# Kernel optimization log

Hardware: AMD Instinct MI355X
Metric: run time of the kernel (lower is better)

## Reference

```python
import jax, jax.numpy as jnp
import numpy as np

D_MODEL = 1024
N_HEADS = 16
HEAD_DIM = D_MODEL // N_HEADS
D_FF = 4096
ROPE_BASE = 10000.0
LN_EPS = 1e-5


def setup_inputs() -> dict:
    key = jax.random.key(0)
    ks = jax.random.split(key, 12)
    B, S = 2, 2048
    s = 0.02
    inp = {
        "x": jax.random.normal(ks[0], (B, S, D_MODEL), dtype=jnp.float32),
        "Wq": jax.random.normal(ks[1], (D_MODEL, D_MODEL), dtype=jnp.float32) * s,
        "bq": jnp.zeros((D_MODEL,), jnp.float32),
        "Wk": jax.random.normal(ks[2], (D_MODEL, D_MODEL), dtype=jnp.float32) * s,
        "bk": jnp.zeros((D_MODEL,), jnp.float32),
        "Wv": jax.random.normal(ks[3], (D_MODEL, D_MODEL), dtype=jnp.float32) * s,
        "bv": jnp.zeros((D_MODEL,), jnp.float32),
        "Wo": jax.random.normal(ks[4], (D_MODEL, D_MODEL), dtype=jnp.float32) * s,
        "bo": jnp.zeros((D_MODEL,), jnp.float32),
        "ln1_g": jnp.ones((D_MODEL,), jnp.float32),
        "ln1_b": jnp.zeros((D_MODEL,), jnp.float32),
        "W1": jax.random.normal(ks[5], (D_MODEL, D_FF), dtype=jnp.float32) * s,
        "b1": jnp.zeros((D_FF,), jnp.float32),
        "W2": jax.random.normal(ks[6], (D_FF, D_MODEL), dtype=jnp.float32) * s,
        "b2": jnp.zeros((D_MODEL,), jnp.float32),
        "ln2_g": jnp.ones((D_MODEL,), jnp.float32),
        "ln2_b": jnp.zeros((D_MODEL,), jnp.float32),
    }
    return inp


def _layernorm(x, g, b):
    mu = jnp.mean(x, axis=-1, keepdims=True)
    var = jnp.var(x, axis=-1, keepdims=True)
    return (x - mu) * jax.lax.rsqrt(var + LN_EPS) * g + b


def _rope_cos_sin(seq_len, dtype):
    inv_freq = 1.0 / (ROPE_BASE ** (jnp.arange(0, HEAD_DIM, 2, dtype=jnp.float32) / HEAD_DIM))
    t = jnp.arange(seq_len, dtype=jnp.float32)
    freqs = jnp.einsum("i,j->ij", t, inv_freq)          # [S, HEAD_DIM/2]
    emb = jnp.concatenate([freqs, freqs], axis=-1)        # [S, HEAD_DIM]
    return jnp.cos(emb).astype(dtype), jnp.sin(emb).astype(dtype)


def _rotate_half(x):
    x1, x2 = jnp.split(x, 2, axis=-1)
    return jnp.concatenate([-x2, x1], axis=-1)


def reference(x, Wq, bq, Wk, bk, Wv, bv, Wo, bo, ln1_g, ln1_b,
              W1, b1, W2, b2, ln2_g, ln2_b):
    B, S, _ = x.shape
    residual = x
    h = _layernorm(x, ln1_g, ln1_b)

    def split_heads(y):  # [B,S,D] -> [B,H,S,hd]
        return y.reshape(B, S, N_HEADS, HEAD_DIM).transpose(0, 2, 1, 3)

    q = split_heads(h @ Wq + bq)
    k = split_heads(h @ Wk + bk)
    v = split_heads(h @ Wv + bv)

    cos, sin = _rope_cos_sin(S, x.dtype)  # [S, hd], broadcast over B,H
    q = q * cos + _rotate_half(q) * sin
    k = k * cos + _rotate_half(k) * sin

    scale = HEAD_DIM ** -0.5
    scores = jnp.einsum("bhqd,bhkd->bhqk", q, k) * scale
    attn = jax.nn.softmax(scores, axis=-1)
    ctx = jnp.einsum("bhqk,bhkd->bhqd", attn, v)           # [B,H,S,hd]
    ctx = ctx.transpose(0, 2, 1, 3).reshape(B, S, D_MODEL)
    attn_out = ctx @ Wo + bo

    x = residual + attn_out
    residual = x
    h = _layernorm(x, ln2_g, ln2_b)
    ffn = jax.nn.gelu(h @ W1 + b1, approximate=False) @ W2 + b2
    return residual + ffn
```

## Files before the change

### kernel.cpp

```cpp
#include <hip/hip_runtime.h>
#include <hip/hip_bf16.h>
#include <stdint.h>

#define S_LEN 2048
#define NH 16
#define HD 64
#define DM 1024
#define DFF 4096
#define MTOK 4096

typedef __attribute__((ext_vector_type(8))) short short8;
typedef __attribute__((ext_vector_type(4))) float f32x4;
typedef unsigned short u16;
typedef unsigned int u32;

__device__ __forceinline__ float bf2f(u16 u) {
  union { u32 i; float f; } x; x.i = ((u32)u) << 16; return x.f;
}
__device__ __forceinline__ u16 f2bf(float f) {
  union { float f; u32 i; } x; x.f = f;
  u32 r = x.i + 0x7fffu + ((x.i >> 16) & 1u);
  return (u16)(r >> 16);
}
__device__ __forceinline__ void gload16(const u16* g, u16* l) {
  __builtin_amdgcn_global_load_lds(
      (__attribute__((address_space(1))) u32*)g,
      (__attribute__((address_space(3))) u32*)l, 16, 0, 0);
}

#define VM0 asm volatile("s_waitcnt vmcnt(0)" ::: "memory")
#define VM6 asm volatile("s_waitcnt vmcnt(6)" ::: "memory")
#define BARR do { __builtin_amdgcn_s_barrier(); asm volatile("" ::: "memory"); } while (0)
#define LGKM0 do { asm volatile("s_waitcnt lgkmcnt(0)" ::: "memory"); __builtin_amdgcn_sched_barrier(0); } while (0)
#define PRIO1 __builtin_amdgcn_s_setprio(1)
#define PRIO0 __builtin_amdgcn_s_setprio(0)

__device__ __forceinline__ void transpose_tile(const float* __restrict__ W,
                                               u16* __restrict__ Wt, int K, int N,
                                               int n0, int k0, int tx, int ty,
                                               float (*tile)[33]) {
#pragma unroll
  for (int i = 0; i < 4; ++i)
    tile[ty + i * 8][tx] = W[(size_t)(k0 + ty + i * 8) * N + n0 + tx];
  __syncthreads();
#pragma unroll
  for (int i = 0; i < 4; ++i)
    Wt[(size_t)(n0 + ty + i * 8) * K + k0 + tx] = f2bf(tile[tx][ty + i * 8]);
}

__global__ __launch_bounds__(256) void prep(
    const float* __restrict__ Wq, const float* __restrict__ Wk,
    const float* __restrict__ Wv, const float* __restrict__ Wo,
    const float* __restrict__ W1, const float* __restrict__ W2,
    u16* __restrict__ WQKVT, u16* __restrict__ WOT, u16* __restrict__ W1T,
    u16* __restrict__ W2T, float* __restrict__ cosT, float* __restrict__ sinT,
    const float* __restrict__ x, const float* __restrict__ g,
    const float* __restrict__ b, u16* __restrict__ H) {
  __shared__ float tile[32][33];
  __shared__ float red[8];
  const int r = blockIdx.x;
  const int t = threadIdx.x;
  const int tx = t & 31, ty = t >> 5;
  if (r < 4096) {
    const float* W = (r < 1024) ? Wq : (r < 2048) ? Wk : (r < 3072) ? Wv : Wo;
    u16* Wt = (r < 1024) ? WQKVT
              : (r < 2048) ? WQKVT + 1024 * 1024
              : (r < 3072) ? WQKVT + 2 * 1024 * 1024 : WOT;
    int sub = r & 1023;
    transpose_tile(W, Wt, 1024, 1024, (sub & 31) * 32, (sub >> 5) * 32, tx, ty, tile);
  } else if (r < 8192) {
    int sub = r - 4096;
    transpose_tile(W1, W1T, 1024, 4096, (sub & 127) * 32, (sub >> 7) * 32, tx, ty, tile);
  } else if (r < 12288) {
    int sub = r - 8192;
    transpose_tile(W2, W2T, 4096, 1024, (sub & 31) * 32, (sub >> 5) * 32, tx, ty, tile);
  } else if (r < 12544) {
    int id = (r - 12288) * 256 + t;
    int s = id >> 5, j = id & 31;
    float inv = powf(10000.0f, -(float)j * (1.0f / 32.0f));
    float fr = (float)s * inv;
    cosT[id] = cosf(fr);
    sinT[id] = sinf(fr);
  } else {
    int row = r - 12544;
    float4 v = ((const float4*)(x + ((size_t)row << 10)))[t];
    float s = v.x + v.y + v.z + v.w;
    float q = v.x * v.x + v.y * v.y + v.z * v.z + v.w * v.w;
#pragma unroll
    for (int m = 1; m < 64; m <<= 1) {
      s += __shfl_xor(s, m, 64);
      q += __shfl_xor(q, m, 64);
    }
    int lane = t & 63, w = t >> 6;
    if (lane == 0) { red[w] = s; red[4 + w] = q; }
    __syncthreads();
    s = red[0] + red[1] + red[2] + red[3];
    q = red[4] + red[5] + red[6] + red[7];
    float mu = s * (1.0f / 1024.0f);
    float var = q * (1.0f / 1024.0f) - mu * mu;
    float rstd = rsqrtf(var + 1e-5f);
    float4 gv = ((const float4*)g)[t];
    float4 bv = ((const float4*)b)[t];
    ushort4 o;
    o.x = f2bf((v.x - mu) * rstd * gv.x + bv.x);
    o.y = f2bf((v.y - mu) * rstd * gv.y + bv.y);
    o.z = f2bf((v.z - mu) * rstd * gv.z + bv.z);
    o.w = f2bf((v.w - mu) * rstd * gv.w + bv.w);
    ((ushort4*)(H + ((size_t)row << 10)))[t] = o;
  }
}

__global__ __launch_bounds__(256) void ln_bf16(const float* __restrict__ x,
                                               const float* __restrict__ g,
                                               const float* __restrict__ b,
                                               u16* __restrict__ out) {
  int row = blockIdx.x;
  int t = threadIdx.x;
  float4 v = ((const float4*)(x + ((size_t)row << 10)))[t];
  float s = v.x + v.y + v.z + v.w;
  float q = v.x * v.x + v.y * v.y + v.z * v.z + v.w * v.w;
#pragma unroll
  for (int m = 1; m < 64; m <<= 1) {
    s += __shfl_xor(s, m, 64);
    q += __shfl_xor(q, m, 64);
  }
  __shared__ float red[8];
  int lane = t & 63, w = t >> 6;
  if (lane == 0) { red[w] = s; red[4 + w] = q; }
  __syncthreads();
  s = red[0] + red[1] + red[2] + red[3];
  q = red[4] + red[5] + red[6] + red[7];
  float mu = s * (1.0f / 1024.0f);
  float var = q * (1.0f / 1024.0f) - mu * mu;
  float rstd = rsqrtf(var + 1e-5f);
  float4 gv = ((const float4*)g)[t];
  float4 bv = ((const float4*)b)[t];
  ushort4 o;
  o.x = f2bf((v.x - mu) * rstd * gv.x + bv.x);
  o.y = f2bf((v.y - mu) * rstd * gv.y + bv.y);
  o.z = f2bf((v.z - mu) * rstd * gv.z + bv.z);
  o.w = f2bf((v.w - mu) * rstd * gv.w + bv.w);
  ((ushort4*)(out + ((size_t)row << 10)))[t] = o;
}

#define MMQ(IB, NB)                                                          \
  _Pragma("unroll") for (int i_ = 0; i_ < 4; ++i_)                           \
  _Pragma("unroll") for (int n_ = 0; n_ < 2; ++n_)                           \
  _Pragma("unroll") for (int k_ = 0; k_ < 2; ++k_)                           \
    acc[(IB) + i_][(NB) + n_] = __builtin_amdgcn_mfma_f32_16x16x32_bf16(     \
        a[i_][k_], b[(NB) + n_][k_], acc[(IB) + i_][(NB) + n_], 0, 0, 0);

template <int EPI>
__global__ __launch_bounds__(512, 2) void gemm256(
    const u16* __restrict__ A, const u16* __restrict__ Bt, int N, int K,
    const float* __restrict__ bias, const float* __restrict__ bq,
    const float* __restrict__ bk, const float* __restrict__ bv,
    const float* __restrict__ cosT, const float* __restrict__ sinT,
    u16* __restrict__ d0, u16* __restrict__ d1, u16* __restrict__ d2) {
  __shared__ __align__(16) u16 As[2][256 * 64];
  __shared__ __align__(16) u16 Bs[2][256 * 64];
  const int t = threadIdx.x;
  const int lane = t & 63, wid = t >> 6;
  const int fr = lane & 15, fq = lane >> 4;
  const int m0 = blockIdx.y << 8, n0 = blockIdx.x << 8;
  const int wmo = (wid >> 2) << 7;
  const int wno = (wid & 3) << 6;
  const int r7 = fr & 7;
  const int srow = t >> 3, ssl = t & 7;

  f32x4 acc[8][4];
#pragma unroll
  for (int i = 0; i < 8; ++i)
#pragma unroll
    for (int n = 0; n < 4; ++n) acc[i][n] = (f32x4){0.f, 0.f, 0.f, 0.f};

  short8 a[4][2], b[4][2];

  auto stageA = [&](int slot, int kt) {
#pragma unroll
    for (int c = 0; c < 4; ++c) {
      const int row = (c << 6) + srow;
      gload16(A + (size_t)(m0 + row) * K + kt + ((ssl ^ (row & 7)) << 3),
              &As[slot][(size_t)((c << 9) + t) << 3]);
    }
  };
  auto stageB = [&](int slot, int kt) {
#pragma unroll
    for (int c = 0; c < 4; ++c) {
      const int row = (c << 6) + srow;
      gload16(Bt + (size_t)(n0 + row) * K + kt + ((ssl ^ (row & 7)) << 3),
              &Bs[slot][(size_t)((c << 9) + t) << 3]);
    }
  };
  auto readA = [&](int slot, int ibase) {
#pragma unroll
    for (int i = 0; i < 4; ++i) {
      const u16* rp = &As[slot][(wmo + ((ibase + i) << 4) + fr) << 6];
      a[i][0] = *(const short8*)(rp + ((fq ^ r7) << 3));
      a[i][1] = *(const short8*)(rp + (((4 + fq) ^ r7) << 3));
    }
  };
  auto readB = [&](int slot, int nbase) {
#pragma unroll
    for (int n = 0; n < 2; ++n) {
      const u16* rp = &Bs[slot][(wno + ((nbase + n) << 4) + fr) << 6];
      b[nbase + n][0] = *(const short8*)(rp + ((fq ^ r7) << 3));
      b[nbase + n][1] = *(const short8*)(rp + (((4 + fq) ^ r7) << 3));
    }
  };

  stageA(0, 0);
  stageB(0, 0);
  const int iters = K >> 7;
  for (int it = 0; it < iters; ++it) {
    const int kt = it << 7;
    VM0; BARR;
    readA(0, 0); readB(0, 0);
    stageA(1, kt + 64);
    LGKM0; PRIO1; MMQ(0, 0); PRIO0;
    BARR;
    readB(0, 2);
    stageB(1, kt + 64);
    LGKM0; PRIO1; MMQ(0, 2); PRIO0;
    BARR;
    readA(0, 4);
    LGKM0; PRIO1; MMQ(4, 2); PRIO0;
    BARR;
    PRIO1; MMQ(4, 0); PRIO0;
    VM0; BARR;
    readA(1, 0); readB(1, 0);
    if (it + 1 < iters) stageA(0, kt + 128);
    LGKM0; PRIO1; MMQ(0, 0); PRIO0;
    BARR;
    readB(1, 2);
    if (it + 1 < iters) stageB(0, kt + 128);
    LGKM0; PRIO1; MMQ(0, 2); PRIO0;
    BARR;
    readA(1, 4);
    LGKM0; PRIO1; MMQ(4, 2); PRIO0;
    BARR;
    PRIO1; MMQ(4, 0); PRIO0;
  }

  if (EPI == 0) {
    const int colbase = n0 + wno;
    const int slice = colbase >> 10;
    const int cb = colbase & 1023;
    const int hh = cb >> 6;
    if (slice < 2) {
      const float sc = (slice == 0) ? 0.125f * 1.44269504088896f : 1.0f;
      const float* bb_ = (slice == 0) ? bq : bk;
      u16* dst = (slice == 0) ? d0 : d1;
#pragma unroll
      for (int i = 0; i < 8; ++i) {
        const int row0 = m0 + wmo + (i << 4) + (fq << 2);
#pragma unroll
        for (int n = 0; n < 2; ++n) {
          const int d = n * 16 + fr;
          const float blo = bb_[cb + d];
          const float bhi = bb_[cb + d + 32];
#pragma unroll
          for (int j = 0; j < 4; ++j) {
            const int row = row0 + j;
            const int ss = row & 2047, bb2 = row >> 11;
            const float c = cosT[ss * 32 + d];
            const float sn = sinT[ss * 32 + d];
            const float av = acc[i][n][j] + blo;
            const float bv2 = acc[i][n + 2][j] + bhi;
            const size_t base = ((size_t)((bb2 * 16 + hh) * 2048 + ss)) << 6;
            dst[base + d] = f2bf((av * c - bv2 * sn) * sc);
            dst[base + d + 32] = f2bf((bv2 * c + av * sn) * sc);
          }
        }
      }
    } else {
#pragma unroll
      for (int i = 0; i < 8; ++i) {
        const int row0 = m0 + wmo + (i << 4) + (fq << 2);
#pragma unroll
        for (int n = 0; n < 4; ++n) {
          const int d = n * 16 + fr;
          const float bia = bv[cb + d];
#pragma unroll
          for (int j = 0; j < 4; ++j) {
            const int row = row0 + j;
            const int ss = row & 2047, bb2 = row >> 11;
            d2[((size_t)((bb2 * 16 + hh) * 64 + d)) * 2048 + ss] =
                f2bf(acc[i][n][j] + bia);
          }
        }
      }
    }
  } else {
#pragma unroll
    for (int i = 0; i < 8; ++i) {
      const int row0 = m0 + wmo + (i << 4) + (fq << 2);
#pragma unroll
      for (int n = 0; n < 4; ++n) {
        const int col = n0 + wno + n * 16 + fr;
        const float bia = bias[col];
#pragma unroll
        for (int j = 0; j < 4; ++j) {
          const int row = row0 + j;
          const float v = acc[i][n][j] + bia;
          const float gl = 0.5f * v * (1.0f + erff(v * 0.70710678118f));
          d0[(size_t)row * N + col] = f2bf(gl);
        }
      }
    }
  }
}

__global__ __launch_bounds__(256, 2) void gemm_bt2(
    const u16* __restrict__ A, const u16* __restrict__ Bt, int K,
    const float* __restrict__ bias, const float* __restrict__ resid,
    float* __restrict__ dst) {
  __shared__ __align__(16) u16 As[3][128 * 64];
  __shared__ __align__(16) u16 Bs[3][64 * 64];
  const int t = threadIdx.x, lane = t & 63, wid = t >> 6;
  const int fr = lane & 15, fq = lane >> 4;
  const int bid = blockIdx.x;
  const int xcd = bid & 7, within = bid >> 3;
  const int m0 = (xcd * 4 + (within >> 4)) << 7;
  const int n0 = (within & 15) << 6;
  const int wm = (wid >> 1) << 6;
  const int wn = (wid & 1) << 5;
  const int sr = t >> 3, sl = t & 7;
  const int sw7 = fr & 7;

  f32x4 acc[4][2];
#pragma unroll
  for (int i = 0; i < 4; ++i)
#pragma unroll
    for (int n = 0; n < 2; ++n) acc[i][n] = (f32x4){0.f, 0.f, 0.f, 0.f};

  auto stage = [&](int b, int kt) {
#pragma unroll
    for (int c = 0; c < 4; ++c) {
      int R = c * 32 + sr;
      gload16(A + (size_t)(m0 + R) * K + kt + ((sl ^ (R & 7)) << 3),
              &As[b][R * 64 + sl * 8]);
    }
#pragma unroll
    for (int c = 0; c < 2; ++c) {
      int R = c * 32 + sr;
      gload16(Bt + (size_t)(n0 + R) * K + kt + ((sl ^ (R & 7)) << 3),
              &Bs[b][R * 64 + sl * 8]);
    }
  };

  stage(0, 0);
  stage(1, 64);
  const int iters = K >> 6;
  for (int it = 0; it < iters; ++it) {
    if (it + 1 < iters) { VM6; } else { VM0; }
    BARR;
    if (it + 2 < iters) stage((it + 2) % 3, (it + 2) << 6);
    const int slot = it % 3;
    short8 a[4][2], b[2][2];
#pragma unroll
    for (int i = 0; i < 4; ++i) {
      const char* rp = (const char*)&As[slot][(wm + i * 16 + fr) * 64];
      a[i][0] = *(const short8*)(rp + ((fq ^ sw7) << 4));
      a[i][1] = *(const short8*)(rp + (((4 + fq) ^ sw7) << 4));
    }
#pragma unroll
    for (int n = 0; n < 2; ++n) {
      const char* rp = (const char*)&Bs[slot][(wn + n * 16 + fr) * 64];
      b[n][0] = *(const short8*)(rp + ((fq ^ sw7) << 4));
      b[n][1] = *(const short8*)(rp + (((4 + fq) ^ sw7) << 4));
    }
    PRIO1;
#pragma unroll
    for (int i = 0; i < 4; ++i)
#pragma unroll
      for (int n = 0; n < 2; ++n)
#pragma unroll
        for (int k2 = 0; k2 < 2; ++k2)
          acc[i][n] = __builtin_amdgcn_mfma_f32_16x16x32_bf16(a[i][k2], b[n][k2],
                                                              acc[i][n], 0, 0, 0);
    PRIO0;
  }

#pragma unroll
  for (int i = 0; i < 4; ++i) {
    int row0 = m0 + wm + i * 16 + (fq << 2);
#pragma unroll
    for (int n = 0; n < 2; ++n) {
      int col = n0 + wn + n * 16 + fr;
      float bia = bias[col];
#pragma unroll
      for (int j = 0; j < 4; ++j) {
        size_t idx = (size_t)(row0 + j) * 1024 + col;
        dst[idx] = acc[i][n][j] + bia + resid[idx];
      }
    }
  }
}

__global__ __launch_bounds__(512, 4) void attn_fwd(const u16* __restrict__ q,
                                                   const u16* __restrict__ k,
                                                   const u16* __restrict__ vt,
                                                   u16* __restrict__ ctx) {
  __shared__ __align__(16) u16 Ks[2][64 * 64];
  __shared__ __align__(16) u16 Vs[2][64 * 64];
  __shared__ __align__(16) u16 Pb[8][16 * 64];
  const int t = threadIdx.x, lane = t & 63, w = t >> 6;
  const int fr = lane & 15, fq = lane >> 4;
  const int bid = blockIdx.x;
  const int bh = (bid & 7) * 4 + ((bid >> 3) & 3);
  const int qt = bid >> 5;
  const int q0w = qt * 128 + w * 16;
  const size_t hbase = (size_t)bh << 17;
  const u16* kg = k + hbase;
  const u16* vg = vt + hbase;
  const int sr = t >> 3;
  const int sl = t & 7;
  const int sw7 = fr & 7;

  short8 aq0, aq1;
  {
    const u16* qp = q + hbase + (size_t)(q0w + fr) * 64 + fq * 8;
    aq0 = *(const short8*)qp;
    aq1 = *(const short8*)(qp + 32);
  }

  float lacc = 0.f;
  f32x4 o[4];
#pragma unroll
  for (int n = 0; n < 4; ++n) o[n] = (f32x4){0.f, 0.f, 0.f, 0.f};

  auto stage = [&](int buf, int kt) {
    int gs = sl ^ (sr & 7);
    gload16(kg + (size_t)(kt + sr) * 64 + gs * 8, &Ks[buf][sr * 64 + sl * 8]);
    gload16(vg + (size_t)sr * 2048 + kt + gs * 8, &Vs[buf][sr * 64 + sl * 8]);
  };

  stage(0, 0);
  int buf = 0;
  for (int it = 0; it < 32; ++it) {
    VM0;
    BARR;
    if (it < 31) stage(buf ^ 1, (it + 1) * 64);

    f32x4 s[4];
    const char* kbase = (const char*)&Ks[buf][0];
    PRIO1;
#pragma unroll
    for (int n = 0; n < 4; ++n) {
      const char* kr = kbase + (n * 16 + fr) * 128;
      short8 kb0 = *(const short8*)(kr + ((fq ^ sw7) << 4));
      short8 kb1 = *(const short8*)(kr + (((4 + fq) ^ sw7) << 4));
      s[n] = (f32x4){0.f, 0.f, 0.f, 0.f};
      s[n] = __builtin_amdgcn_mfma_f32_16x16x32_bf16(kb0, aq0, s[n], 0, 0, 0);
      s[n] = __builtin_amdgcn_mfma_f32_16x16x32_bf16(kb1, aq1, s[n], 0, 0, 0);
    }
    PRIO0;

    char* pw = (char*)&Pb[w][0];
#pragma unroll
    for (int n = 0; n < 4; ++n) {
      float p0 = exp2f(s[n][0]);
      float p1 = exp2f(s[n][1]);
      float p2 = exp2f(s[n][2]);
      float p3 = exp2f(s[n][3]);
      lacc += (p0 + p1) + (p2 + p3);
      u32 d0, d1;
      asm volatile("v_cvt_pk_bf16_f32 %0, %1, %2" : "=v"(d0) : "v"(p0), "v"(p1));
      asm volatile("v_cvt_pk_bf16_f32 %0, %1, %2" : "=v"(d1) : "v"(p2), "v"(p3));
      int off = fr * 128 + ((n * 32 + fq * 8) ^ (sw7 << 4));
      *(uint2*)(pw + off) = make_uint2(d0, d1);
    }

    LGKM0;
    const char* prd = (const char*)&Pb[w][0];
    short8 ap0 = *(const short8*)(prd + fr * 128 + ((fq ^ sw7) << 4));
    short8 ap1 = *(const short8*)(prd + fr * 128 + (((4 + fq) ^ sw7) << 4));

    const char* vbase = (const char*)&Vs[buf][0];
    PRIO1;
#pragma unroll
    for (int n = 0; n < 4; ++n) {
      const char* vr = vbase + (n * 16 + fr) * 128;
      short8 vb0 = *(const short8*)(vr + ((fq ^ sw7) << 4));
      short8 vb1 = *(const short8*)(vr + (((4 + fq) ^ sw7) << 4));
      o[n] = __builtin_amdgcn_mfma_f32_16x16x32_bf16(ap0, vb0, o[n], 0, 0, 0);
      o[n] = __builtin_amdgcn_mfma_f32_16x16x32_bf16(ap1, vb1, o[n], 0, 0, 0);
    }
    PRIO0;
    buf ^= 1;
  }

  lacc += __shfl_xor(lacc, 16, 64);
  lacc += __shfl_xor(lacc, 32, 64);

  const int bb = bh >> 4, hh = bh & 15;
  float rl[4];
#pragma unroll
  for (int j = 0; j < 4; ++j) rl[j] = 1.0f / __shfl(lacc, fq * 4 + j, 64);
#pragma unroll
  for (int n = 0; n < 4; ++n) {
    int d = n * 16 + fr;
#pragma unroll
    for (int j = 0; j < 4; ++j) {
      int row = q0w + fq * 4 + j;
      ctx[(((size_t)(bb * 2048 + row)) << 10) + hh * 64 + d] = f2bf(o[n][j] * rl[j]);
    }
  }
}

extern "C" void kernel_launch(void* const* d_in, const int* in_sizes, int n_in,
                              void* d_out, int out_size, void* d_ws, size_t ws_size,
                              hipStream_t stream) {
  const float* x    = (const float*)d_in[0];
  const float* Wq   = (const float*)d_in[1];
  const float* bq   = (const float*)d_in[2];
  const float* Wk   = (const float*)d_in[3];
  const float* bk   = (const float*)d_in[4];
  const float* Wv   = (const float*)d_in[5];
  const float* bv   = (const float*)d_in[6];
  const float* Wo   = (const float*)d_in[7];
  const float* bo   = (const float*)d_in[8];
  const float* ln1g = (const float*)d_in[9];
  const float* ln1b = (const float*)d_in[10];
  const float* W1   = (const float*)d_in[11];
  const float* b1   = (const float*)d_in[12];
  const float* W2   = (const float*)d_in[13];
  const float* b2   = (const float*)d_in[14];
  const float* ln2g = (const float*)d_in[15];
  const float* ln2b = (const float*)d_in[16];

  char* ws = (char*)d_ws;
  size_t off = 0;
  auto alloc = [&](size_t bytes) {
    char* p = ws + off;
    off += (bytes + 1023) & ~(size_t)1023;
    return p;
  };
  u16* WQKVT = (u16*)alloc((size_t)3 * DM * DM * 2);
  u16* WOT = (u16*)alloc((size_t)DM * DM * 2);
  u16* W1T = (u16*)alloc((size_t)DFF * DM * 2);
  u16* W2T = (u16*)alloc((size_t)DM * DFF * 2);
  float* COS = (float*)alloc((size_t)S_LEN * 32 * 4);
  float* SIN = (float*)alloc((size_t)S_LEN * 32 * 4);
  u16* H   = (u16*)alloc((size_t)MTOK * DM * 2);
  u16* Qb  = (u16*)alloc((size_t)MTOK * DM * 2);
  u16* Kb  = (u16*)alloc((size_t)MTOK * DM * 2);
  u16* VT  = (u16*)alloc((size_t)MTOK * DM * 2);
  u16* CTX = (u16*)alloc((size_t)MTOK * DM * 2);
  float* X2 = (float*)alloc((size_t)MTOK * DM * 4);
  u16* FFN1 = Qb;
  if (ws_size < off) return;

  dim3 blk256(256);
  prep<<<dim3(16640), blk256, 0, stream>>>(Wq, Wk, Wv, Wo, W1, W2, WQKVT, WOT,
                                           W1T, W2T, COS, SIN, x, ln1g, ln1b, H);
  gemm256<0><<<dim3(12, 16), dim3(512), 0, stream>>>(
      H, WQKVT, 3072, 1024, nullptr, bq, bk, bv, COS, SIN, Qb, Kb, VT);
  attn_fwd<<<dim3(512), dim3(512), 0, stream>>>(Qb, Kb, VT, CTX);
  gemm_bt2<<<dim3(512), blk256, 0, stream>>>(CTX, WOT, 1024, bo, x, X2);
  ln_bf16<<<4096, blk256, 0, stream>>>(X2, ln2g, ln2b, H);
  gemm256<1><<<dim3(16, 16), dim3(512), 0, stream>>>(
      H, W1T, 4096, 1024, b1, nullptr, nullptr, nullptr, nullptr, nullptr,
      FFN1, nullptr, nullptr);
  gemm_bt2<<<dim3(512), blk256, 0, stream>>>(FFN1, W2T, 4096, b2, X2, (float*)d_out);
}
```

Before: 243.4 us.

## Rewrite attention with 32x32x16 MFMA and register-resident P via permlane32 swap

The attention kernel moves from 16x16x32 to 32x32x16 bf16 MFMA. Each wave now owns 32 query rows, and blocks shrink from 512 to 256 threads. The softmax probabilities are repacked into the A-operand layout in registers using permlane32_swap, which removes the per-wave LDS round trip for P and its wait. This is meant to cut LDS traffic and instruction count and to raise MFMA efficiency. In exchange it needs more registers per thread and puts fewer waves per block to hide the K/V staging latency.

```diff
diff --git a/kernel.cpp b/kernel.cpp
--- a/kernel.cpp
+++ b/kernel.cpp
@@ -11,6 +11,8 @@
 
 typedef __attribute__((ext_vector_type(8))) short short8;
 typedef __attribute__((ext_vector_type(4))) float f32x4;
+typedef __attribute__((ext_vector_type(16))) float f32x16;
+typedef __attribute__((ext_vector_type(2))) int i32x2;
 typedef unsigned short u16;
 typedef unsigned int u32;
 
@@ -398,42 +400,52 @@
   }
 }
 
-__global__ __launch_bounds__(512, 4) void attn_fwd(const u16* __restrict__ q,
+__global__ __launch_bounds__(256, 4) void attn_fwd(const u16* __restrict__ q,
                                                    const u16* __restrict__ k,
                                                    const u16* __restrict__ vt,
                                                    u16* __restrict__ ctx) {
   __shared__ __align__(16) u16 Ks[2][64 * 64];
   __shared__ __align__(16) u16 Vs[2][64 * 64];
-  __shared__ __align__(16) u16 Pb[8][16 * 64];
+  __shared__ float Lr[4][32];
   const int t = threadIdx.x, lane = t & 63, w = t >> 6;
-  const int fr = lane & 15, fq = lane >> 4;
+  const int ql = lane & 31;
+  const int h = lane >> 5;
   const int bid = blockIdx.x;
   const int bh = (bid & 7) * 4 + ((bid >> 3) & 3);
   const int qt = bid >> 5;
-  const int q0w = qt * 128 + w * 16;
+  const int q0w = qt * 128 + w * 32;
   const size_t hbase = (size_t)bh << 17;
   const u16* kg = k + hbase;
   const u16* vg = vt + hbase;
   const int sr = t >> 3;
   const int sl = t & 7;
-  const int sw7 = fr & 7;
-
-  short8 aq0, aq1;
-  {
-    const u16* qp = q + hbase + (size_t)(q0w + fr) * 64 + fq * 8;
-    aq0 = *(const short8*)qp;
-    aq1 = *(const short8*)(qp + 32);
-  }
+  const int l7 = lane & 7;
+
+  short8 qf[4];
+#pragma unroll
+  for (int f = 0; f < 4; ++f)
+    qf[f] = *(const short8*)(q + hbase + (size_t)(q0w + ql) * 64 + f * 16 + h * 8);
 
   float lacc = 0.f;
-  f32x4 o[4];
-#pragma unroll
-  for (int n = 0; n < 4; ++n) o[n] = (f32x4){0.f, 0.f, 0.f, 0.f};
+  f32x16 o[2];
+#pragma unroll
+  for (int db = 0; db < 2; ++db)
+#pragma unroll
+    for (int r = 0; r < 16; ++r) o[db][r] = 0.f;
 
   auto stage = [&](int buf, int kt) {
-    int gs = sl ^ (sr & 7);
-    gload16(kg + (size_t)(kt + sr) * 64 + gs * 8, &Ks[buf][sr * 64 + sl * 8]);
-    gload16(vg + (size_t)sr * 2048 + kt + gs * 8, &Vs[buf][sr * 64 + sl * 8]);
+#pragma unroll
+    for (int c = 0; c < 2; ++c) {
+      int R = c * 32 + sr;
+      int gs = sl ^ (R & 7);
+      gload16(kg + (size_t)(kt + R) * 64 + gs * 8, &Ks[buf][R * 64 + sl * 8]);
+    }
+#pragma unroll
+    for (int c = 0; c < 2; ++c) {
+      int R = c * 32 + sr;
+      int gs = sl ^ (R & 7);
+      gload16(vg + (size_t)R * 2048 + kt + gs * 8, &Vs[buf][R * 64 + sl * 8]);
+    }
   };
 
   stage(0, 0);
@@ -443,69 +455,78 @@
     BARR;
     if (it < 31) stage(buf ^ 1, (it + 1) * 64);
 
-    f32x4 s[4];
-    const char* kbase = (const char*)&Ks[buf][0];
+    f32x16 s[2];
     PRIO1;
 #pragma unroll
-    for (int n = 0; n < 4; ++n) {
-      const char* kr = kbase + (n * 16 + fr) * 128;
-      short8 kb0 = *(const short8*)(kr + ((fq ^ sw7) << 4));
-      short8 kb1 = *(const short8*)(kr + (((4 + fq) ^ sw7) << 4));
-      s[n] = (f32x4){0.f, 0.f, 0.f, 0.f};
-      s[n] = __builtin_amdgcn_mfma_f32_16x16x32_bf16(kb0, aq0, s[n], 0, 0, 0);
-      s[n] = __builtin_amdgcn_mfma_f32_16x16x32_bf16(kb1, aq1, s[n], 0, 0, 0);
+    for (int kb = 0; kb < 2; ++kb) {
+#pragma unroll
+      for (int r = 0; r < 16; ++r) s[kb][r] = 0.f;
+#pragma unroll
+      for (int f = 0; f < 4; ++f) {
+        const u16* kr = &Ks[buf][(kb * 32 + ql) * 64 + (((2 * f + h) ^ l7) << 3)];
+        s[kb] = __builtin_amdgcn_mfma_f32_32x32x16_bf16(*(const short8*)kr, qf[f],
+                                                        s[kb], 0, 0, 0);
+      }
     }
     PRIO0;
 
-    char* pw = (char*)&Pb[w][0];
-#pragma unroll
-    for (int n = 0; n < 4; ++n) {
-      float p0 = exp2f(s[n][0]);
-      float p1 = exp2f(s[n][1]);
-      float p2 = exp2f(s[n][2]);
-      float p3 = exp2f(s[n][3]);
-      lacc += (p0 + p1) + (p2 + p3);
-      u32 d0, d1;
-      asm volatile("v_cvt_pk_bf16_f32 %0, %1, %2" : "=v"(d0) : "v"(p0), "v"(p1));
-      asm volatile("v_cvt_pk_bf16_f32 %0, %1, %2" : "=v"(d1) : "v"(p2), "v"(p3));
-      int off = fr * 128 + ((n * 32 + fq * 8) ^ (sw7 << 4));
-      *(uint2*)(pw + off) = make_uint2(d0, d1);
-    }
-
-    LGKM0;
-    const char* prd = (const char*)&Pb[w][0];
-    short8 ap0 = *(const short8*)(prd + fr * 128 + ((fq ^ sw7) << 4));
-    short8 ap1 = *(const short8*)(prd + fr * 128 + (((4 + fq) ^ sw7) << 4));
-
-    const char* vbase = (const char*)&Vs[buf][0];
+    float p[2][16];
+#pragma unroll
+    for (int kb = 0; kb < 2; ++kb)
+#pragma unroll
+      for (int r = 0; r < 16; ++r) {
+        p[kb][r] = exp2f(s[kb][r]);
+        lacc += p[kb][r];
+      }
+
+    short8 pf[4];
+#pragma unroll
+    for (int kb = 0; kb < 2; ++kb)
+#pragma unroll
+      for (int rrp = 0; rrp < 2; ++rrp) {
+        u32 y0, y1, x0, x1;
+        asm volatile("v_cvt_pk_bf16_f32 %0, %1, %2" : "=v"(y0)
+                     : "v"(p[kb][8 * rrp + 0]), "v"(p[kb][8 * rrp + 1]));
+        asm volatile("v_cvt_pk_bf16_f32 %0, %1, %2" : "=v"(y1)
+                     : "v"(p[kb][8 * rrp + 2]), "v"(p[kb][8 * rrp + 3]));
+        asm volatile("v_cvt_pk_bf16_f32 %0, %1, %2" : "=v"(x0)
+                     : "v"(p[kb][8 * rrp + 4]), "v"(p[kb][8 * rrp + 5]));
+        asm volatile("v_cvt_pk_bf16_f32 %0, %1, %2" : "=v"(x1)
+                     : "v"(p[kb][8 * rrp + 6]), "v"(p[kb][8 * rrp + 7]));
+        i32x2 r0 = __builtin_amdgcn_permlane32_swap((int)x0, (int)y0, false, false);
+        i32x2 r1 = __builtin_amdgcn_permlane32_swap((int)x1, (int)y1, false, false);
+        u32 dw[4] = {(u32)r0[1], (u32)r1[1], (u32)r0[0], (u32)r1[0]};
+        pf[kb * 2 + rrp] = *(short8*)dw;
+      }
+
     PRIO1;
 #pragma unroll
-    for (int n = 0; n < 4; ++n) {
-      const char* vr = vbase + (n * 16 + fr) * 128;
-      short8 vb0 = *(const short8*)(vr + ((fq ^ sw7) << 4));
-      short8 vb1 = *(const short8*)(vr + (((4 + fq) ^ sw7) << 4));
-      o[n] = __builtin_amdgcn_mfma_f32_16x16x32_bf16(ap0, vb0, o[n], 0, 0, 0);
-      o[n] = __builtin_amdgcn_mfma_f32_16x16x32_bf16(ap1, vb1, o[n], 0, 0, 0);
+    for (int db = 0; db < 2; ++db) {
+#pragma unroll
+      for (int f = 0; f < 4; ++f) {
+        const u16* vr = &Vs[buf][(db * 32 + ql) * 64 + (((2 * f + h) ^ l7) << 3)];
+        o[db] = __builtin_amdgcn_mfma_f32_32x32x16_bf16(pf[f], *(const short8*)vr,
+                                                        o[db], 0, 0, 0);
+      }
     }
     PRIO0;
     buf ^= 1;
   }
 
-  lacc += __shfl_xor(lacc, 16, 64);
   lacc += __shfl_xor(lacc, 32, 64);
+  Lr[w][ql] = 1.0f / lacc;
+  LGKM0;
 
   const int bb = bh >> 4, hh = bh & 15;
-  float rl[4];
-#pragma unroll
-  for (int j = 0; j < 4; ++j) rl[j] = 1.0f / __shfl(lacc, fq * 4 + j, 64);
-#pragma unroll
-  for (int n = 0; n < 4; ++n) {
-    int d = n * 16 + fr;
-#pragma unroll
-    for (int j = 0; j < 4; ++j) {
-      int row = q0w + fq * 4 + j;
-      ctx[(((size_t)(bb * 2048 + row)) << 10) + hh * 64 + d] = f2bf(o[n][j] * rl[j]);
-    }
+#pragma unroll
+  for (int r = 0; r < 16; ++r) {
+    const int qr = (r & 3) + 8 * (r >> 2) + 4 * h;
+    const float rl = Lr[w][qr];
+    const int row = q0w + qr;
+    const size_t base = (((size_t)(bb * 2048 + row)) << 10) + hh * 64;
+#pragma unroll
+    for (int db = 0; db < 2; ++db)
+      ctx[base + db * 32 + ql] = f2bf(o[db][r] * rl);
   }
 }
 
@@ -557,7 +578,7 @@
                                            W1T, W2T, COS, SIN, x, ln1g, ln1b, H);
   gemm256<0><<<dim3(12, 16), dim3(512), 0, stream>>>(
       H, WQKVT, 3072, 1024, nullptr, bq, bk, bv, COS, SIN, Qb, Kb, VT);
-  attn_fwd<<<dim3(512), dim3(512), 0, stream>>>(Qb, Kb, VT, CTX);
+  attn_fwd<<<dim3(512), blk256, 0, stream>>>(Qb, Kb, VT, CTX);
   gemm_bt2<<<dim3(512), blk256, 0, stream>>>(CTX, WOT, 1024, bo, x, X2);
   ln_bf16<<<4096, blk256, 0, stream>>>(X2, ln2g, ln2b, H);
   gemm256<1><<<dim3(16, 16), dim3(512), 0, stream>>>(
```

Result: no change. 246.1 us (+1.1%).
